# Optimization experiments

Hardware: AMD Instinct MI355X
Metric: run time of the kernel (lower is better)

Reference implementation:

```python
import jax, jax.numpy as jnp
import numpy as np
from jax import lax

DN = ('NCHW', 'OIHW', 'NCHW')

def conv(x, w, b):
    y = lax.conv_general_dilated(x, w, (1, 1), 'VALID', dimension_numbers=DN)
    return y + b[None, :, None, None]

def maxpool2(x):
    return lax.reduce_window(x, -jnp.inf, lax.max, (1, 1, 2, 2), (1, 1, 2, 2), 'VALID')

def setup_inputs() -> dict:
    key = jax.random.key(0)
    ks = jax.random.split(key, 16)
    s = 0.05
    return {
        'x': jax.random.normal(ks[0], (8192, 1, 28, 28), jnp.float32),
        'kf_w1': jax.random.normal(ks[1], (8, 1, 7, 7), jnp.float32) * s,
        'kf_b1': jax.random.normal(ks[2], (8,), jnp.float32) * s,
        'kf_w2': jax.random.normal(ks[3], (10, 8, 5, 5), jnp.float32) * s,
        'kf_b2': jax.random.normal(ks[4], (10,), jnp.float32) * s,
        'kf_fc1_w': jax.random.normal(ks[5], (32, 90), jnp.float32) * s,
        'kf_fc1_b': jax.random.normal(ks[6], (32,), jnp.float32) * s,
        'kf_fc2_w': jax.random.normal(ks[7], (40, 32), jnp.float32) * s,
        'kf_fc2_b': jax.random.normal(ks[8], (40,), jnp.float32) * s,
        'conv2_w': jax.random.normal(ks[9], (20, 10, 5, 5), jnp.float32) * s,
        'conv2_b': jax.random.normal(ks[10], (20,), jnp.float32) * s,
        'fc1_w': jax.random.normal(ks[11], (50, 320), jnp.float32) * s,
        'fc1_b': jax.random.normal(ks[12], (50,), jnp.float32) * s,
        'fc2_w': jax.random.normal(ks[13], (10, 50), jnp.float32) * s,
        'fc2_b': jax.random.normal(ks[14], (10,), jnp.float32) * s,
    }

def _forward(x, kf_w1, kf_b1, kf_w2, kf_b2, kf_fc1_w, kf_fc1_b, kf_fc2_w, kf_fc2_b,
             conv2_w, conv2_b, fc1_w, fc1_b, fc2_w, fc2_b):
    n = x.shape[0]
    # KernelFinder: conv7 -> pool -> relu -> conv5 -> pool -> relu
    f = jax.nn.relu(maxpool2(conv(x, kf_w1, kf_b1)))        # [N,8,11,11]
    f = jax.nn.relu(maxpool2(conv(f, kf_w2, kf_b2)))        # [N,10,3,3]
    f = f.reshape(n, 90)
    h = jax.nn.relu(f @ kf_fc1_w.T + kf_fc1_b)
    kernels = (h @ kf_fc2_w.T + kf_fc2_b).reshape(n, 10, 1, 2, 2)
    # per-sample dynamic conv: each image gets its own [10,1,2,2] kernel
    def one(img, k):
        return lax.conv_general_dilated(img[None], k, (1, 1), 'VALID',
                                        dimension_numbers=DN)[0]
    y = jax.vmap(one)(x, kernels)                           # [N,10,27,27]
    y = jax.nn.relu(maxpool2(y))                            # [N,10,13,13]
    # dropout2d is identity in eval mode
    y = jax.nn.relu(maxpool2(conv(y, conv2_w, conv2_b)))    # [N,20,4,4]
    y = y.reshape(n, 320)
    y = jax.nn.relu(y @ fc1_w.T + fc1_b)
    # F.dropout identity in eval
    y = y @ fc2_w.T + fc2_b
    return jax.nn.log_softmax(y, axis=1)

def reference(x, kf_w1, kf_b1, kf_w2, kf_b2, kf_fc1_w, kf_fc1_b, kf_fc2_w, kf_fc2_b,
              conv2_w, conv2_b, fc1_w, fc1_b, fc2_w, fc2_b):
    return _forward(x, kf_w1, kf_b1, kf_w2, kf_b2, kf_fc1_w, kf_fc1_b, kf_fc2_w,
                    kf_fc2_b, conv2_w, conv2_b, fc1_w, fc1_b, fc2_w, fc2_b)
```

## Files before the change

kernel.cpp:

```cpp
#include <hip/hip_runtime.h>
#include <math.h>

#define TPB 192

typedef __attribute__((ext_vector_type(8))) short bf16x8;
typedef __attribute__((ext_vector_type(4))) float f32x4;

#define OX    0
#define OXB0  784
#define OXB1  1264
#define OXI   1744
#define OC7   4816
#define OC1B  6736
#define OC5   1744
#define OY2   784
#define OF    2704
#define OH    2796
#define OK2   2828
#define OC2S  2868
#define OP3   0
#define OPF   320
#define OA1   420
#define OZ    472
#define SM_TOT 7264

#define W3U 0
#define W5U 9600
#define W7U 13184
#define WSU_TOT 14208

__device__ __forceinline__ unsigned short f2bf(float f) {
    unsigned int u = __float_as_uint(f);
    u += 0x7FFF + ((u >> 16) & 1);
    return (unsigned short)(u >> 16);
}

__global__ void repack_w(const float* __restrict__ conv2_w,
                         const float* __restrict__ kf_w2,
                         const float* __restrict__ kf_w1,
                         unsigned short* __restrict__ ws)
{
    int i = blockIdx.x * blockDim.x + threadIdx.x;
    if (i < 9600) {
        int g = i / 640, rem = i % 640;
        int oc = rem >> 5, k = rem & 31;
        int kyp = g % 3, kx = g / 3;
        int kyip = k >> 4, ic = k & 15, ky = 2 * kyp + kyip;
        float v = 0.f;
        if (ic < 10 && ky < 5)
            v = conv2_w[(oc * 10 + ic) * 25 + ky * 5 + kx];
        ws[W3U + i] = f2bf(v);
    } else if (i < 13184) {
        int j = i - 9600;
        int s = j >> 9, rem = j & 511;
        int oc = rem >> 5, k = rem & 31;
        int tap = 4 * s + (k >> 3), ic = k & 7;
        float v = 0.f;
        if (oc < 10 && tap < 25)
            v = kf_w2[(oc * 8 + ic) * 25 + tap];
        ws[W5U + j] = f2bf(v);
    } else if (i < WSU_TOT) {
        int j = i - 13184;
        int s = j >> 9, oc = (j >> 5) & 15, k = j & 31;
        int ky = s * 4 + (k >> 3), kx = k & 7;
        float v = 0.f;
        if (oc < 8 && kx < 7 && ky < 7)
            v = kf_w1[oc * 49 + ky * 7 + kx];
        ws[W7U + j] = f2bf(v);
    }
}

__global__ __launch_bounds__(TPB) void fused_forward(
    const float* __restrict__ x,
    const float* __restrict__ kf_w1, const float* __restrict__ kf_b1,
    const float* __restrict__ kf_w2, const float* __restrict__ kf_b2,
    const float* __restrict__ kf_fc1_w, const float* __restrict__ kf_fc1_b,
    const float* __restrict__ kf_fc2_w, const float* __restrict__ kf_fc2_b,
    const float* __restrict__ conv2_w, const float* __restrict__ conv2_b,
    const float* __restrict__ fc1_w, const float* __restrict__ fc1_b,
    const float* __restrict__ fc2_w, const float* __restrict__ fc2_b,
    const unsigned short* __restrict__ wsu,
    float* __restrict__ out)
{
    __shared__ __align__(16) float sm[SM_TOT];
    const int tid = threadIdx.x;
    const int n = blockIdx.x;

    const float bias1 = kf_b1[tid & 7];

    {
        const float4* xg = (const float4*)(x + (long long)n * 784);
        float4* d = (float4*)&sm[OX];
        for (int i = tid; i < 196; i += TPB) d[i] = xg[i];
        float4* z4 = (float4*)&sm[OXB0];
        for (int i = tid; i < 240; i += TPB) z4[i] = float4{0.f, 0.f, 0.f, 0.f};
    }
    __syncthreads();

    if (tid < 196) {
        float4 v = *(const float4*)&sm[OX + tid * 4];
        unsigned short* b0 = (unsigned short*)&sm[OXB0];
        unsigned short* b1 = (unsigned short*)&sm[OXB1];
        #pragma unroll
        for (int j = 0; j < 4; ++j) {
            int e = tid * 4 + j;
            int row = e / 28, c = e - row * 28;
            unsigned short bv = f2bf(((const float*)&v)[j]);
            int pos = row * 32 + c;
            b0[pos] = bv;
            if (pos > 0) b1[pos - 1] = bv;
        }
    }
    __syncthreads();

    auto stageXi = [&](int it) {
        unsigned short* Xi = (unsigned short*)&sm[OXI];
        const int* b0 = (const int*)&sm[OXB0];
        const int* b1 = (const int*)&sm[OXB1];
        #pragma unroll
        for (int i = 0; i < 4; ++i) {
            int t = tid + 192 * i;
            int nn = t % 96, ky = t / 96;
            int pp = nn >= 48 ? 1 : 0;
            int rem = nn - pp * 48;
            int rr = rem >= 24 ? 1 : 0;
            int col = rem - rr * 24;
            int row = 4 * it + 2 * pp + rr + ky;
            row = row > 29 ? 29 : row;
            const int* src = (col & 1) ? (b1 + row * 16 + (col >> 1))
                                       : (b0 + row * 16 + (col >> 1));
            int4 w4;
            w4.x = src[0]; w4.y = src[1]; w4.z = src[2]; w4.w = src[3];
            *(int4*)(Xi + nn * 64 + ((ky * 8) ^ ((nn & 7) << 3))) = w4;
        }
    };

    stageXi(0);
    __syncthreads();

    for (int it = 0; it < 6; ++it) {
        {
            const int wv = tid >> 6, l = tid & 63;
            const int lm = l & 15, lk = l >> 4;
            const unsigned short* Xi = (const unsigned short*)&sm[OXI];
            const unsigned short* W7 = wsu + W7U;
            const int n0 = wv * 16 + lm, n1 = n0 + 48;
            f32x4 acc0 = {0.f, 0.f, 0.f, 0.f};
            f32x4 acc1 = {0.f, 0.f, 0.f, 0.f};
            #pragma unroll
            for (int s = 0; s < 2; ++s) {
                bf16x8 A = *(const bf16x8*)(W7 + s * 512 + lm * 32 + lk * 8);
                bf16x8 B0 = *(const bf16x8*)(Xi + n0 * 64 + ((s * 32 + lk * 8) ^ ((n0 & 7) << 3)));
                bf16x8 B1 = *(const bf16x8*)(Xi + n1 * 64 + ((s * 32 + lk * 8) ^ ((n1 & 7) << 3)));
                acc0 = __builtin_amdgcn_mfma_f32_16x16x32_bf16(A, B0, acc0, 0, 0, 0);
                acc1 = __builtin_amdgcn_mfma_f32_16x16x32_bf16(A, B1, acc1, 0, 0, 0);
            }
            float* C7 = &sm[OC7];
            *(f32x4*)(C7 + n0 * 20 + lk * 4) = acc0;
            *(f32x4*)(C7 + n1 * 20 + lk * 4) = acc1;
        }
        __syncthreads();

        if (it < 5) stageXi(it + 1);
        if (tid < 176) {
            int oc = tid & 7, r = tid >> 3;
            int c = r % 11, pp = r / 11;
            int p = 2 * it + pp;
            if (p < 11) {
                const float* C7 = &sm[OC7];
                int nb = pp * 48 + 2 * c;
                float v00 = C7[nb * 20 + oc];
                float v01 = C7[(nb + 1) * 20 + oc];
                float v10 = C7[(nb + 24) * 20 + oc];
                float v11 = C7[(nb + 25) * 20 + oc];
                float m = fmaxf(fmaxf(v00, v01), fmaxf(v10, v11)) + bias1;
                ((unsigned short*)&sm[OC1B])[p * 96 + c * 8 + oc] = f2bf(fmaxf(m, 0.f));
            }
        }
        __syncthreads();
    }

    {
        const int wv = tid >> 6, l = tid & 63;
        const int lm = l & 15, lq = l >> 4;
        int nn = wv * 16 + lm;
        int nc = nn > 35 ? 35 : nn;
        const int rr = nc / 6, cc = nc - rr * 6;
        const unsigned short* c1b = (const unsigned short*)&sm[OC1B];
        const char* W5 = (const char*)(wsu + W5U);
        f32x4 acc = {0.f, 0.f, 0.f, 0.f};
        #pragma unroll
        for (int s = 0; s < 7; ++s) {
            int tap = 4 * s + lq;
            int ky = (tap * 13) >> 6;
            int kx = tap - ky * 5;
            bf16x8 A = *(const bf16x8*)(W5 + s * 1024 + lm * 64 + lq * 16);
            bf16x8 B = *(const bf16x8*)(c1b + (rr + ky) * 96 + (cc + kx) * 8);
            acc = __builtin_amdgcn_mfma_f32_16x16x32_bf16(A, B, acc, 0, 0, 0);
        }
        *(f32x4*)(&sm[OC5] + nn * 20 + lq * 4) = acc;
    }
    __syncthreads();

    if (tid < 90) {
        int oc = tid % 10, rr = tid / 10;
        int py = rr / 3, px = rr % 3;
        const float* C5 = &sm[OC5];
        int nb = (2 * py) * 6 + 2 * px;
        float v = fmaxf(fmaxf(C5[nb * 20 + oc], C5[(nb + 1) * 20 + oc]),
                        fmaxf(C5[(nb + 6) * 20 + oc], C5[(nb + 7) * 20 + oc]));
        sm[OF + oc * 9 + rr] = fmaxf(v + kf_b2[oc], 0.f);
    }
    __syncthreads();

    if (tid < 32) {
        float acc = kf_fc1_b[tid];
        const float2* wr = (const float2*)&kf_fc1_w[tid * 90];
        const float2* ff = (const float2*)&sm[OF];
        for (int i = 0; i < 45; ++i) {
            float2 wv = wr[i], fv = ff[i];
            acc = fmaf(wv.x, fv.x, acc);
            acc = fmaf(wv.y, fv.y, acc);
        }
        sm[OH + tid] = fmaxf(acc, 0.f);
    }
    if (tid < 40) {
        float acc = kf_fc2_b[tid];
        const float4* wr = (const float4*)&kf_fc2_w[tid * 32];
        const float4* hh = (const float4*)&sm[OH];
        #pragma unroll
        for (int i = 0; i < 8; ++i) {
            float4 wv = wr[i], hv = hh[i];
            acc = fmaf(wv.x, hv.x, acc);
            acc = fmaf(wv.y, hv.y, acc);
            acc = fmaf(wv.z, hv.z, acc);
            acc = fmaf(wv.w, hv.w, acc);
        }
        sm[OK2 + tid] = acc;
    }
    if (tid >= 64) {
        float4* z4 = (float4*)&sm[OY2];
        for (int i = tid - 64; i < 468; i += 128) z4[i] = float4{0.f, 0.f, 0.f, 0.f};
    }
    __syncthreads();

    if (tid < 120) {
        int oc = tid % 10, py = tid / 10;
        float4 kv = *(const float4*)&sm[OK2 + oc * 4];
        float k0 = kv.x, k1 = kv.y, k2 = kv.z, k3 = kv.w;
        const float* x0 = &sm[OX + 2 * py * 28];
        const float* x1 = x0 + 28;
        const float* x2 = x0 + 56;
        float2 q0 = *(const float2*)&x0[0];
        float2 q1 = *(const float2*)&x1[0];
        float2 q2 = *(const float2*)&x2[0];
        float A0 = q0.x, B0 = q0.y;
        float A1 = q1.x, B1 = q1.y;
        float A2 = q2.x, B2 = q2.y;
        unsigned short* y2 = (unsigned short*)&sm[OY2];
        #pragma unroll
        for (int j = 0; j < 12; ++j) {
            float2 r0 = *(const float2*)&x0[2 * j + 2];
            float2 r1 = *(const float2*)&x1[2 * j + 2];
            float2 r2v = *(const float2*)&x2[2 * j + 2];
            float C0 = r0.x, C1 = r1.x, C2 = r2v.x;
            float c00 = A0 * k0 + B0 * k1 + A1 * k2 + B1 * k3;
            float c01 = B0 * k0 + C0 * k1 + B1 * k2 + C1 * k3;
            float c10 = A1 * k0 + B1 * k1 + A2 * k2 + B2 * k3;
            float c11 = B1 * k0 + C1 * k1 + B2 * k2 + C2 * k3;
            float m = fmaxf(fmaxf(c00, c01), fmaxf(c10, c11));
            y2[py * 288 + j * 24 + oc] = f2bf(fmaxf(m, 0.f));
            A0 = C0; A1 = C1; A2 = C2;
            B0 = r0.y; B1 = r1.y; B2 = r2v.y;
        }
    }
    __syncthreads();

    {
        const int wv = tid >> 6;
        if (wv < 2) {
            const int l  = tid & 63;
            const int lm = l & 15, lk = l >> 4;
            f32x4 a00 = {0.f, 0.f, 0.f, 0.f};
            f32x4 a01 = a00, a10 = a00, a11 = a00;
            const char* W3 = (const char*)(wsu + W3U);
            const int aoff0 = lm * 64 + lk * 16;
            const int oc1 = 16 + (lm < 4 ? lm : 3);
            const int aoff1 = oc1 * 64 + lk * 16;
            const int n0 = wv * 32 + lm;
            const int n1 = n0 + 16;
            const int kyip = l >> 5, icb = (lk & 1) * 8;
            const unsigned short* Y2 = (const unsigned short*)&sm[OY2];
            const int b0 = ((n0 >> 3) + kyip) * 288 + (n0 & 7) * 24 + icb;
            const int b1 = ((n1 >> 3) + kyip) * 288 + (n1 & 7) * 24 + icb;
            #pragma unroll
            for (int p = 0; p < 3; ++p) {
                #pragma unroll
                for (int kx = 0; kx < 5; ++kx) {
                    const char* wa = W3 + (kx * 3 + p) * 1280;
                    bf16x8 A0 = *(const bf16x8*)(wa + aoff0);
                    bf16x8 A1 = *(const bf16x8*)(wa + aoff1);
                    const int bo = p * 576 + kx * 24;
                    bf16x8 B0 = *(const bf16x8*)(Y2 + b0 + bo);
                    bf16x8 B1 = *(const bf16x8*)(Y2 + b1 + bo);
                    a00 = __builtin_amdgcn_mfma_f32_16x16x32_bf16(A0, B0, a00, 0, 0, 0);
                    a01 = __builtin_amdgcn_mfma_f32_16x16x32_bf16(A0, B1, a01, 0, 0, 0);
                    a10 = __builtin_amdgcn_mfma_f32_16x16x32_bf16(A1, B0, a10, 0, 0, 0);
                    a11 = __builtin_amdgcn_mfma_f32_16x16x32_bf16(A1, B1, a11, 0, 0, 0);
                }
            }
            float* C = &sm[OC2S];
            *(f32x4*)(C + n0 * 36 + lk * 4)      = a00;
            *(f32x4*)(C + n1 * 36 + lk * 4)      = a01;
            *(f32x4*)(C + n0 * 36 + 16 + lk * 4) = a10;
            *(f32x4*)(C + n1 * 36 + 16 + lk * 4) = a11;
        }
    }
    __syncthreads();

    if (tid < 80) {
        int oc = tid % 20, py = tid / 20;
        float b = conv2_b[oc];
        const float* C = &sm[OC2S];
        #pragma unroll
        for (int px = 0; px < 4; ++px) {
            int n00 = (2 * py) * 8 + 2 * px;
            float c00 = C[n00 * 36 + oc];
            float c01 = C[(n00 + 1) * 36 + oc];
            float c10 = C[(n00 + 8) * 36 + oc];
            float c11 = C[(n00 + 9) * 36 + oc];
            float m = fmaxf(fmaxf(c00, c01), fmaxf(c10, c11)) + b;
            sm[OP3 + oc * 16 + py * 4 + px] = fmaxf(m, 0.f);
        }
    }
    __syncthreads();

    if (tid < 100) {
        int g = tid / 50, o = tid % 50;
        const float4* wr4 = (const float4*)&fc1_w[o * 320 + g * 160];
        const float4* pp4 = (const float4*)&sm[OP3 + g * 160];
        float acc = 0.f;
        for (int i = 0; i < 40; ++i) {
            float4 wv = wr4[i], pv = pp4[i];
            acc = fmaf(wv.x, pv.x, acc);
            acc = fmaf(wv.y, pv.y, acc);
            acc = fmaf(wv.z, pv.z, acc);
            acc = fmaf(wv.w, pv.w, acc);
        }
        sm[OPF + tid] = acc;
    }
    __syncthreads();

    if (tid < 50) {
        float acc = fc1_b[tid] + sm[OPF + tid] + sm[OPF + 50 + tid];
        sm[OA1 + tid] = fmaxf(acc, 0.f);
    }
    if (tid < 10) {
        float acc = fc2_b[tid];
        const float2* wr = (const float2*)&fc2_w[tid * 50];
        #pragma unroll
        for (int i = 0; i < 25; ++i) {
            float2 wv = wr[i];
            acc = fmaf(wv.x, sm[OA1 + 2 * i], acc);
            acc = fmaf(wv.y, sm[OA1 + 2 * i + 1], acc);
        }
        sm[OZ + tid] = acc;
    }
    if (tid < 10) {
        float m = sm[OZ + 0];
        #pragma unroll
        for (int i = 1; i < 10; ++i) m = fmaxf(m, sm[OZ + i]);
        float s = 0.f;
        #pragma unroll
        for (int i = 0; i < 10; ++i) s += expf(sm[OZ + i] - m);
        out[n * 10 + tid] = sm[OZ + tid] - m - logf(s);
    }
}

extern "C" void kernel_launch(void* const* d_in, const int* in_sizes, int n_in,
                              void* d_out, int out_size, void* d_ws, size_t ws_size,
                              hipStream_t stream) {
    const float* x        = (const float*)d_in[0];
    const float* kf_w1    = (const float*)d_in[1];
    const float* kf_b1    = (const float*)d_in[2];
    const float* kf_w2    = (const float*)d_in[3];
    const float* kf_b2    = (const float*)d_in[4];
    const float* kf_fc1_w = (const float*)d_in[5];
    const float* kf_fc1_b = (const float*)d_in[6];
    const float* kf_fc2_w = (const float*)d_in[7];
    const float* kf_fc2_b = (const float*)d_in[8];
    const float* conv2_w  = (const float*)d_in[9];
    const float* conv2_b  = (const float*)d_in[10];
    const float* fc1_w    = (const float*)d_in[11];
    const float* fc1_b    = (const float*)d_in[12];
    const float* fc2_w    = (const float*)d_in[13];
    const float* fc2_b    = (const float*)d_in[14];

    const int N = in_sizes[0] / 784;

    unsigned short* wsu = (unsigned short*)d_ws;
    repack_w<<<(WSU_TOT + 255) / 256, 256, 0, stream>>>(conv2_w, kf_w2, kf_w1, wsu);

    fused_forward<<<N, TPB, 0, stream>>>(
        x, kf_w1, kf_b1, kf_w2, kf_b2, kf_fc1_w, kf_fc1_b, kf_fc2_w, kf_fc2_b,
        conv2_w, conv2_b, fc1_w, fc1_b, fc2_w, fc2_b, wsu, (float*)d_out);
}
```

Before: 247.5 us.

## Read conv7 MFMA operands directly from shifted bf16 image copies, drop im2col staging

The first 7x7 convolution used to build an explicit swizzled im2col buffer every iteration, in six iterations with two MFMA tiles each. It now builds four column-shifted bf16 copies of the padded image once and loads the B operands straight from them. It also runs three groups of four tiles per wave and hoists the conv7 weight fragments into registers. This removes the per-iteration staging pass, cuts the number of barriers and shrinks shared memory, which may raise occupancy. In exchange it uses unaligned 8-byte LDS loads with possible bank conflicts and computes some padded or unused columns.

```diff
diff --git a/kernel.cpp b/kernel.cpp
--- a/kernel.cpp
+++ b/kernel.cpp
@@ -7,22 +7,20 @@
 typedef __attribute__((ext_vector_type(4))) float f32x4;
 
 #define OX    0
-#define OXB0  784
-#define OXB1  1264
-#define OXI   1744
-#define OC7   4816
-#define OC1B  6736
-#define OC5   1744
+#define OXB   784
+#define OC7   2720
+#define OC1B  5024
+#define OC5   784
 #define OY2   784
-#define OF    2704
-#define OH    2796
-#define OK2   2828
-#define OC2S  2868
+#define OC2S  2720
+#define OF    5552
+#define OH    5644
+#define OK2   5676
 #define OP3   0
 #define OPF   320
 #define OA1   420
 #define OZ    472
-#define SM_TOT 7264
+#define SM_TOT 5716
 
 #define W3U 0
 #define W5U 9600
@@ -87,102 +85,90 @@
     const int n = blockIdx.x;
 
     const float bias1 = kf_b1[tid & 7];
+    const int l  = tid & 63, wv = tid >> 6;
+    const int lm = l & 15, lk = l >> 4;
+
+    bf16x8 A7_0, A7_1;
+    {
+        const unsigned short* W7 = wsu + W7U;
+        A7_0 = *(const bf16x8*)(W7 + lm * 32 + lk * 8);
+        A7_1 = *(const bf16x8*)(W7 + 512 + lm * 32 + lk * 8);
+    }
 
     {
         const float4* xg = (const float4*)(x + (long long)n * 784);
         float4* d = (float4*)&sm[OX];
         for (int i = tid; i < 196; i += TPB) d[i] = xg[i];
-        float4* z4 = (float4*)&sm[OXB0];
-        for (int i = tid; i < 240; i += TPB) z4[i] = float4{0.f, 0.f, 0.f, 0.f};
-    }
-    __syncthreads();
-
-    if (tid < 196) {
-        float4 v = *(const float4*)&sm[OX + tid * 4];
-        unsigned short* b0 = (unsigned short*)&sm[OXB0];
-        unsigned short* b1 = (unsigned short*)&sm[OXB1];
-        #pragma unroll
-        for (int j = 0; j < 4; ++j) {
-            int e = tid * 4 + j;
-            int row = e / 28, c = e - row * 28;
-            unsigned short bv = f2bf(((const float*)&v)[j]);
-            int pos = row * 32 + c;
-            b0[pos] = bv;
-            if (pos > 0) b1[pos - 1] = bv;
-        }
-    }
-    __syncthreads();
-
-    auto stageXi = [&](int it) {
-        unsigned short* Xi = (unsigned short*)&sm[OXI];
-        const int* b0 = (const int*)&sm[OXB0];
-        const int* b1 = (const int*)&sm[OXB1];
-        #pragma unroll
-        for (int i = 0; i < 4; ++i) {
-            int t = tid + 192 * i;
-            int nn = t % 96, ky = t / 96;
-            int pp = nn >= 48 ? 1 : 0;
-            int rem = nn - pp * 48;
-            int rr = rem >= 24 ? 1 : 0;
-            int col = rem - rr * 24;
-            int row = 4 * it + 2 * pp + rr + ky;
-            row = row > 29 ? 29 : row;
-            const int* src = (col & 1) ? (b1 + row * 16 + (col >> 1))
-                                       : (b0 + row * 16 + (col >> 1));
-            int4 w4;
-            w4.x = src[0]; w4.y = src[1]; w4.z = src[2]; w4.w = src[3];
-            *(int4*)(Xi + nn * 64 + ((ky * 8) ^ ((nn & 7) << 3))) = w4;
-        }
-    };
-
-    stageXi(0);
-    __syncthreads();
-
-    for (int it = 0; it < 6; ++it) {
+    }
+    __syncthreads();
+
+    {
+        unsigned short* xb = (unsigned short*)&sm[OXB];
+        #pragma unroll
+        for (int i = 0; i < 20; ++i) {
+            int e = i * 192 + tid;
+            int s = e / 960, rem = e - s * 960;
+            int r = rem >> 5, m = rem & 31;
+            int c = m + s;
+            float v = (r < 28 && c < 28) ? sm[OX + r * 28 + c] : 0.f;
+            xb[s * 968 + rem] = f2bf(v);
+        }
+    }
+    __syncthreads();
+
+    for (int g = 0; g < 3; ++g) {
         {
-            const int wv = tid >> 6, l = tid & 63;
-            const int lm = l & 15, lk = l >> 4;
-            const unsigned short* Xi = (const unsigned short*)&sm[OXI];
-            const unsigned short* W7 = wsu + W7U;
-            const int n0 = wv * 16 + lm, n1 = n0 + 48;
-            f32x4 acc0 = {0.f, 0.f, 0.f, 0.f};
-            f32x4 acc1 = {0.f, 0.f, 0.f, 0.f};
+            const unsigned short* xb = (const unsigned short*)&sm[OXB];
+            float* C7 = &sm[OC7];
             #pragma unroll
-            for (int s = 0; s < 2; ++s) {
-                bf16x8 A = *(const bf16x8*)(W7 + s * 512 + lm * 32 + lk * 8);
-                bf16x8 B0 = *(const bf16x8*)(Xi + n0 * 64 + ((s * 32 + lk * 8) ^ ((n0 & 7) << 3)));
-                bf16x8 B1 = *(const bf16x8*)(Xi + n1 * 64 + ((s * 32 + lk * 8) ^ ((n1 & 7) << 3)));
-                acc0 = __builtin_amdgcn_mfma_f32_16x16x32_bf16(A, B0, acc0, 0, 0, 0);
-                acc1 = __builtin_amdgcn_mfma_f32_16x16x32_bf16(A, B1, acc1, 0, 0, 0);
+            for (int j = 0; j < 4; ++j) {
+                int nn = (wv * 4 + j) * 16 + lm;
+                int lr = nn / 24, c = nn - lr * 24;
+                int s = c & 3, q = c - s;
+                f32x4 acc = {0.f, 0.f, 0.f, 0.f};
+                #pragma unroll
+                for (int s4 = 0; s4 < 2; ++s4) {
+                    int rb = 8 * g + lr + s4 * 4 + lk;
+                    rb = rb > 29 ? 29 : rb;
+                    const unsigned short* p = xb + s * 968 + rb * 32 + q;
+                    short4 lo = *(const short4*)p;
+                    short4 hi = *(const short4*)(p + 4);
+                    bf16x8 B;
+                    B[0] = lo.x; B[1] = lo.y; B[2] = lo.z; B[3] = lo.w;
+                    B[4] = hi.x; B[5] = hi.y; B[6] = hi.z; B[7] = hi.w;
+                    acc = __builtin_amdgcn_mfma_f32_16x16x32_bf16(
+                        s4 ? A7_1 : A7_0, B, acc, 0, 0, 0);
+                }
+                if (lk < 2)
+                    *(f32x4*)(C7 + nn * 12 + lk * 4) = acc;
             }
-            float* C7 = &sm[OC7];
-            *(f32x4*)(C7 + n0 * 20 + lk * 4) = acc0;
-            *(f32x4*)(C7 + n1 * 20 + lk * 4) = acc1;
         }
         __syncthreads();
 
-        if (it < 5) stageXi(it + 1);
         if (tid < 176) {
-            int oc = tid & 7, r = tid >> 3;
-            int c = r % 11, pp = r / 11;
-            int p = 2 * it + pp;
-            if (p < 11) {
-                const float* C7 = &sm[OC7];
-                int nb = pp * 48 + 2 * c;
-                float v00 = C7[nb * 20 + oc];
-                float v01 = C7[(nb + 1) * 20 + oc];
-                float v10 = C7[(nb + 24) * 20 + oc];
-                float v11 = C7[(nb + 25) * 20 + oc];
-                float m = fmaxf(fmaxf(v00, v01), fmaxf(v10, v11)) + bias1;
-                ((unsigned short*)&sm[OC1B])[p * 96 + c * 8 + oc] = f2bf(fmaxf(m, 0.f));
+            int oc = tid & 7, qq = tid >> 3;
+            int c = qq % 11, plr2 = qq / 11;
+            const float* C7 = &sm[OC7];
+            unsigned short* c1b = (unsigned short*)&sm[OC1B];
+            #pragma unroll
+            for (int hh = 0; hh < 2; ++hh) {
+                int plr = plr2 + 2 * hh;
+                int p = 4 * g + plr;
+                if (p < 11) {
+                    int nb = (2 * plr) * 24 + 2 * c;
+                    float v00 = C7[nb * 12 + oc];
+                    float v01 = C7[(nb + 1) * 12 + oc];
+                    float v10 = C7[(nb + 24) * 12 + oc];
+                    float v11 = C7[(nb + 25) * 12 + oc];
+                    float m = fmaxf(fmaxf(v00, v01), fmaxf(v10, v11)) + bias1;
+                    c1b[p * 96 + c * 8 + oc] = f2bf(fmaxf(m, 0.f));
+                }
             }
         }
         __syncthreads();
     }
 
     {
-        const int wv = tid >> 6, l = tid & 63;
-        const int lm = l & 15, lq = l >> 4;
         int nn = wv * 16 + lm;
         int nc = nn > 35 ? 35 : nn;
         const int rr = nc / 6, cc = nc - rr * 6;
@@ -191,14 +177,14 @@
         f32x4 acc = {0.f, 0.f, 0.f, 0.f};
         #pragma unroll
         for (int s = 0; s < 7; ++s) {
-            int tap = 4 * s + lq;
+            int tap = 4 * s + lk;
             int ky = (tap * 13) >> 6;
             int kx = tap - ky * 5;
-            bf16x8 A = *(const bf16x8*)(W5 + s * 1024 + lm * 64 + lq * 16);
+            bf16x8 A = *(const bf16x8*)(W5 + s * 1024 + lm * 64 + lk * 16);
             bf16x8 B = *(const bf16x8*)(c1b + (rr + ky) * 96 + (cc + kx) * 8);
             acc = __builtin_amdgcn_mfma_f32_16x16x32_bf16(A, B, acc, 0, 0, 0);
         }
-        *(f32x4*)(&sm[OC5] + nn * 20 + lq * 4) = acc;
+        *(f32x4*)(&sm[OC5] + nn * 20 + lk * 4) = acc;
     }
     __syncthreads();
 
@@ -218,9 +204,9 @@
         const float2* wr = (const float2*)&kf_fc1_w[tid * 90];
         const float2* ff = (const float2*)&sm[OF];
         for (int i = 0; i < 45; ++i) {
-            float2 wv = wr[i], fv = ff[i];
-            acc = fmaf(wv.x, fv.x, acc);
-            acc = fmaf(wv.y, fv.y, acc);
+            float2 wv2 = wr[i], fv = ff[i];
+            acc = fmaf(wv2.x, fv.x, acc);
+            acc = fmaf(wv2.y, fv.y, acc);
         }
         sm[OH + tid] = fmaxf(acc, 0.f);
     }
@@ -230,11 +216,11 @@
         const float4* hh = (const float4*)&sm[OH];
         #pragma unroll
         for (int i = 0; i < 8; ++i) {
-            float4 wv = wr[i], hv = hh[i];
-            acc = fmaf(wv.x, hv.x, acc);
-            acc = fmaf(wv.y, hv.y, acc);
-            acc = fmaf(wv.z, hv.z, acc);
-            acc = fmaf(wv.w, hv.w, acc);
+            float4 wv2 = wr[i], hv = hh[i];
+            acc = fmaf(wv2.x, hv.x, acc);
+            acc = fmaf(wv2.y, hv.y, acc);
+            acc = fmaf(wv2.z, hv.z, acc);
+            acc = fmaf(wv2.w, hv.w, acc);
         }
         sm[OK2 + tid] = acc;
     }
@@ -276,45 +262,40 @@
     }
     __syncthreads();
 
-    {
-        const int wv = tid >> 6;
-        if (wv < 2) {
-            const int l  = tid & 63;
-            const int lm = l & 15, lk = l >> 4;
-            f32x4 a00 = {0.f, 0.f, 0.f, 0.f};
-            f32x4 a01 = a00, a10 = a00, a11 = a00;
-            const char* W3 = (const char*)(wsu + W3U);
-            const int aoff0 = lm * 64 + lk * 16;
-            const int oc1 = 16 + (lm < 4 ? lm : 3);
-            const int aoff1 = oc1 * 64 + lk * 16;
-            const int n0 = wv * 32 + lm;
-            const int n1 = n0 + 16;
-            const int kyip = l >> 5, icb = (lk & 1) * 8;
-            const unsigned short* Y2 = (const unsigned short*)&sm[OY2];
-            const int b0 = ((n0 >> 3) + kyip) * 288 + (n0 & 7) * 24 + icb;
-            const int b1 = ((n1 >> 3) + kyip) * 288 + (n1 & 7) * 24 + icb;
+    if (wv < 2) {
+        f32x4 a00 = {0.f, 0.f, 0.f, 0.f};
+        f32x4 a01 = a00, a10 = a00, a11 = a00;
+        const char* W3 = (const char*)(wsu + W3U);
+        const int aoff0 = lm * 64 + lk * 16;
+        const int oc1 = 16 + (lm < 4 ? lm : 3);
+        const int aoff1 = oc1 * 64 + lk * 16;
+        const int n0 = wv * 32 + lm;
+        const int n1 = n0 + 16;
+        const int kyip = l >> 5, icb = (lk & 1) * 8;
+        const unsigned short* Y2 = (const unsigned short*)&sm[OY2];
+        const int b0 = ((n0 >> 3) + kyip) * 288 + (n0 & 7) * 24 + icb;
+        const int b1 = ((n1 >> 3) + kyip) * 288 + (n1 & 7) * 24 + icb;
+        #pragma unroll
+        for (int p = 0; p < 3; ++p) {
             #pragma unroll
-            for (int p = 0; p < 3; ++p) {
-                #pragma unroll
-                for (int kx = 0; kx < 5; ++kx) {
-                    const char* wa = W3 + (kx * 3 + p) * 1280;
-                    bf16x8 A0 = *(const bf16x8*)(wa + aoff0);
-                    bf16x8 A1 = *(const bf16x8*)(wa + aoff1);
-                    const int bo = p * 576 + kx * 24;
-                    bf16x8 B0 = *(const bf16x8*)(Y2 + b0 + bo);
-                    bf16x8 B1 = *(const bf16x8*)(Y2 + b1 + bo);
-                    a00 = __builtin_amdgcn_mfma_f32_16x16x32_bf16(A0, B0, a00, 0, 0, 0);
-                    a01 = __builtin_amdgcn_mfma_f32_16x16x32_bf16(A0, B1, a01, 0, 0, 0);
-                    a10 = __builtin_amdgcn_mfma_f32_16x16x32_bf16(A1, B0, a10, 0, 0, 0);
-                    a11 = __builtin_amdgcn_mfma_f32_16x16x32_bf16(A1, B1, a11, 0, 0, 0);
-                }
+            for (int kx = 0; kx < 5; ++kx) {
+                const char* wa = W3 + (kx * 3 + p) * 1280;
+                bf16x8 A0 = *(const bf16x8*)(wa + aoff0);
+                bf16x8 A1 = *(const bf16x8*)(wa + aoff1);
+                const int bo = p * 576 + kx * 24;
+                bf16x8 B0 = *(const bf16x8*)(Y2 + b0 + bo);
+                bf16x8 B1 = *(const bf16x8*)(Y2 + b1 + bo);
+                a00 = __builtin_amdgcn_mfma_f32_16x16x32_bf16(A0, B0, a00, 0, 0, 0);
+                a01 = __builtin_amdgcn_mfma_f32_16x16x32_bf16(A0, B1, a01, 0, 0, 0);
+                a10 = __builtin_amdgcn_mfma_f32_16x16x32_bf16(A1, B0, a10, 0, 0, 0);
+                a11 = __builtin_amdgcn_mfma_f32_16x16x32_bf16(A1, B1, a11, 0, 0, 0);
             }
-            float* C = &sm[OC2S];
-            *(f32x4*)(C + n0 * 36 + lk * 4)      = a00;
-            *(f32x4*)(C + n1 * 36 + lk * 4)      = a01;
-            *(f32x4*)(C + n0 * 36 + 16 + lk * 4) = a10;
-            *(f32x4*)(C + n1 * 36 + 16 + lk * 4) = a11;
-        }
+        }
+        float* C = &sm[OC2S];
+        *(f32x4*)(C + n0 * 36 + lk * 4)      = a00;
+        *(f32x4*)(C + n1 * 36 + lk * 4)      = a01;
+        *(f32x4*)(C + n0 * 36 + 16 + lk * 4) = a10;
+        *(f32x4*)(C + n1 * 36 + 16 + lk * 4) = a11;
     }
     __syncthreads();
 
@@ -341,11 +322,11 @@
         const float4* pp4 = (const float4*)&sm[OP3 + g * 160];
         float acc = 0.f;
         for (int i = 0; i < 40; ++i) {
-            float4 wv = wr4[i], pv = pp4[i];
-            acc = fmaf(wv.x, pv.x, acc);
-            acc = fmaf(wv.y, pv.y, acc);
-            acc = fmaf(wv.z, pv.z, acc);
-            acc = fmaf(wv.w, pv.w, acc);
+            float4 wv2 = wr4[i], pv = pp4[i];
+            acc = fmaf(wv2.x, pv.x, acc);
+            acc = fmaf(wv2.y, pv.y, acc);
+            acc = fmaf(wv2.z, pv.z, acc);
+            acc = fmaf(wv2.w, pv.w, acc);
         }
         sm[OPF + tid] = acc;
     }
@@ -360,9 +341,9 @@
         const float2* wr = (const float2*)&fc2_w[tid * 50];
         #pragma unroll
         for (int i = 0; i < 25; ++i) {
-            float2 wv = wr[i];
-            acc = fmaf(wv.x, sm[OA1 + 2 * i], acc);
-            acc = fmaf(wv.y, sm[OA1 + 2 * i + 1], acc);
+            float2 wv2 = wr[i];
+            acc = fmaf(wv2.x, sm[OA1 + 2 * i], acc);
+            acc = fmaf(wv2.y, sm[OA1 + 2 * i + 1], acc);
         }
         sm[OZ + tid] = acc;
     }
```

Measured after the change: 217.7 us (median of 2 runs). -12.0%, faster.
